# Optimization experiments

Measured on AMD Instinct MI355X. Metric: run time of the kernel, lower is better.

The kernel has to match this reference:

```python
import math
import jax, jax.numpy as jnp
import numpy as np

L, D, H, DFF, T, B, BUCKETS = 4, 512, 8, 2048, 256, 8, 32
DH = D // H


def _ln(x, g, b, eps=1e-6):
    m = x.mean(-1, keepdims=True)
    v = ((x - m) ** 2).mean(-1, keepdims=True)
    return (x - m) / jnp.sqrt(v + eps) * g + b


def setup_inputs() -> dict:
    key = jax.random.key(0)
    ki = iter(jax.random.split(key, 32))
    p = lambda shape: jax.random.normal(next(ki), shape, jnp.float32) * 0.02
    inp = {}
    inp['src'] = jax.random.normal(next(ki), (T, B, D), jnp.float32)
    inp['lengths'] = jax.random.randint(next(ki), (B,), 128, T + 1)
    inp['distances'] = jax.random.randint(next(ki), (B, T, T), 0, BUCKETS + 1)
    inp['u'] = jax.random.normal(next(ki), (D,), jnp.float32)
    inp['v'] = jax.random.normal(next(ki), (D,), jnp.float32)
    inp['ln1_g'] = jnp.ones((L, D)); inp['ln1_b'] = jnp.zeros((L, D))
    for nm in ['Wq', 'Wk', 'Wv', 'Wo']:
        inp[nm] = p((L, D, D))
    for nm in ['bq', 'bk', 'bv', 'bo']:
        inp[nm] = jnp.zeros((L, D))
    # learned relative-position embedding table per layer, padding row zeroed
    inp['rel_table'] = p((L, BUCKETS + 1, D)).at[:, BUCKETS, :].set(0.0)
    inp['ffn_ln_g'] = jnp.ones((L, D)); inp['ffn_ln_b'] = jnp.zeros((L, D))
    inp['W1'] = p((L, DFF, D)); inp['b1'] = jnp.zeros((L, DFF))
    inp['W2'] = p((L, D, DFF)); inp['b2'] = jnp.zeros((L, D))
    inp['final_ln_g'] = jnp.ones((D,)); inp['final_ln_b'] = jnp.zeros((D,))
    return inp


def reference(src, lengths, distances, u, v, ln1_g, ln1_b, Wq, bq, Wk, bk, Wv, bv,
              Wo, bo, rel_table, ffn_ln_g, ffn_ln_b, W1, b1, W2, b2,
              final_ln_g, final_ln_b):
    # onmt-style sinusoidal positional encoding with sqrt(d_model) scaling
    pos = jnp.arange(T, dtype=jnp.float32)[:, None]
    div = jnp.exp(jnp.arange(0, D, 2, dtype=jnp.float32) * (-math.log(10000.0) / D))
    pe = jnp.zeros((T, D)).at[:, 0::2].set(jnp.sin(pos * div)).at[:, 1::2].set(jnp.cos(pos * div))
    x = (src * math.sqrt(D) + pe[:, None, :]).transpose(1, 0, 2)  # (B,T,D)
    pad = jnp.arange(T)[None, :] >= lengths[:, None]  # (B,T), True = masked key
    uh = u.reshape(1, H, 1, DH)
    vh = v.reshape(1, H, 1, DH)
    for l in range(L):
        h = _ln(x, ln1_g[l], ln1_b[l])
        def heads(w, b_):
            return (h @ w.T + b_).reshape(B, T, H, DH).transpose(0, 2, 1, 3)
        q = heads(Wq[l], bq[l]) / math.sqrt(DH)  # (B,H,T,DH)
        k = heads(Wk[l], bk[l])
        val = heads(Wv[l], bv[l])
        # content term a_c = (q + u) k^T
        a_c = jnp.einsum('bhqd,bhkd->bhqk', q + uh, k)
        # relative term b_d = (q + v) R^T, R gathered per (query,key) pair
        rel = rel_table[l][distances].reshape(B, T, T, H, DH)  # (B,Q,K,H,DH)
        b_d = jnp.einsum('bhqd,bqkhd->bhqk', q + vh, rel)
        scores = (a_c + b_d).astype(jnp.float32)
        scores = jnp.where(pad[:, None, None, :], -1e18, scores)
        attn = jax.nn.softmax(scores, axis=-1)
        ctx = jnp.einsum('bhqk,bhkd->bhqd', attn, val)
        ctx = ctx.transpose(0, 2, 1, 3).reshape(B, T, D)
        out = ctx @ Wo[l].T + bo[l] + x  # residual (dropout=0)
        # PositionwiseFeedForward: LN -> W1 -> relu -> W2 -> +residual
        h2 = _ln(out, ffn_ln_g[l], ffn_ln_b[l])
        x = jax.nn.relu(h2 @ W1[l].T + b1[l]) @ W2[l].T + b2[l] + out
    x = _ln(x, final_ln_g, final_ln_b)
    return x.transpose(1, 0, 2)  # (T,B,D)
```

## Files before the change

### kernel.cpp

```cpp
#include <hip/hip_runtime.h>
#include <hip/hip_bf16.h>
#include <math.h>

constexpr int L = 4, D = 512, H = 8, DFF = 2048, T = 256, B = 8, BUCKETS = 32;
constexpr int DH = D / H;
constexpr int NT = B * T;
constexpr int QKVLD = 3 * D;

typedef __attribute__((ext_vector_type(8))) short bf16x8;
typedef __attribute__((ext_vector_type(4))) float f32x4;

__device__ __forceinline__ unsigned short f2bf(float f) {
    unsigned int x = __float_as_uint(f);
    return (unsigned short)((x + 0x7fffu + ((x >> 16) & 1u)) >> 16);
}
__device__ __forceinline__ float bf2f(unsigned short u) {
    return __uint_as_float((unsigned int)u << 16);
}

__device__ __forceinline__ void stage16(const unsigned short* g, short* l) {
    __builtin_amdgcn_global_load_lds((const __attribute__((address_space(1))) unsigned int*)g,
                                     (__attribute__((address_space(3))) unsigned int*)l,
                                     16, 0, 0);
}

__global__ __launch_bounds__(256) void embed_kernel(const float* __restrict__ src,
                                                    float* __restrict__ x)
{
    int t = blockIdx.x, tid = threadIdx.x;
    float pe0, pe1;
    {
        int d0 = tid, d1 = tid + 256;
        float dv0 = expf(-(float)(2 * (d0 >> 1)) * (9.210340371976184f / (float)D));
        float dv1 = expf(-(float)(2 * (d1 >> 1)) * (9.210340371976184f / (float)D));
        float a0 = (float)t * dv0, a1 = (float)t * dv1;
        pe0 = (d0 & 1) ? cosf(a0) : sinf(a0);
        pe1 = (d1 & 1) ? cosf(a1) : sinf(a1);
    }
#pragma unroll
    for (int b = 0; b < B; b++) {
        const float* sp = src + ((size_t)t * B + b) * D;
        float* xp = x + ((size_t)(b * T + t)) * D;
        xp[tid]       = sp[tid]       * 22.62741699796952f + pe0;
        xp[tid + 256] = sp[tid + 256] * 22.62741699796952f + pe1;
    }
}

__device__ __forceinline__ void ln_vals(float v0, float v1,
                                        const float* __restrict__ g,
                                        const float* __restrict__ bb,
                                        float* o0, float* o1, int tid)
{
    float s = v0 + v1, q2 = v0 * v0 + v1 * v1;
#pragma unroll
    for (int o = 32; o; o >>= 1) { s += __shfl_xor(s, o); q2 += __shfl_xor(q2, o); }
    __shared__ float rs[4], rq[4];
    int lane = tid & 63, wid = tid >> 6;
    if (lane == 0) { rs[wid] = s; rq[wid] = q2; }
    __syncthreads();
    s = rs[0] + rs[1] + rs[2] + rs[3];
    q2 = rq[0] + rq[1] + rq[2] + rq[3];
    float mean = s * (1.f / (float)D);
    float var = q2 * (1.f / (float)D) - mean * mean;
    float rstd = rsqrtf(var + 1e-6f);
    *o0 = (v0 - mean) * rstd * g[tid] + bb[tid];
    *o1 = (v1 - mean) * rstd * g[tid + 256] + bb[tid + 256];
}

__global__ __launch_bounds__(256) void ln_kernel(const float* __restrict__ x,
                                                 unsigned short* __restrict__ y,
                                                 const float* __restrict__ g,
                                                 const float* __restrict__ bb)
{
    int row = blockIdx.x, tid = threadIdx.x;
    float v0 = x[(size_t)row * D + tid], v1 = x[(size_t)row * D + tid + 256];
    float o0, o1;
    ln_vals(v0, v1, g, bb, &o0, &o1, tid);
    y[(size_t)row * D + tid] = f2bf(o0);
    y[(size_t)row * D + tid + 256] = f2bf(o1);
}

__global__ __launch_bounds__(256) void lnr_kernel(float* __restrict__ X,
                                                  const float* __restrict__ P,
                                                  const float* __restrict__ bias,
                                                  unsigned short* __restrict__ y,
                                                  const float* __restrict__ g,
                                                  const float* __restrict__ bb)
{
    int row = blockIdx.x, tid = threadIdx.x;
    float v0 = X[(size_t)row * D + tid] + bias[tid];
    float v1 = X[(size_t)row * D + tid + 256] + bias[tid + 256];
#pragma unroll
    for (int s = 0; s < 4; s++) {
        v0 += P[((size_t)s * NT + row) * D + tid];
        v1 += P[((size_t)s * NT + row) * D + tid + 256];
    }
    X[(size_t)row * D + tid] = v0;
    X[(size_t)row * D + tid + 256] = v1;
    float o0, o1;
    ln_vals(v0, v1, g, bb, &o0, &o1, tid);
    y[(size_t)row * D + tid] = f2bf(o0);
    y[(size_t)row * D + tid + 256] = f2bf(o1);
}

__global__ __launch_bounds__(256) void final_lnr_kernel(const float* __restrict__ X,
                                                        const float* __restrict__ P,
                                                        const float* __restrict__ bias,
                                                        float* __restrict__ out,
                                                        const float* __restrict__ g,
                                                        const float* __restrict__ bb)
{
    int row = blockIdx.x, tid = threadIdx.x;
    int b = row >> 8, t = row & (T - 1);
    float v0 = X[(size_t)row * D + tid] + bias[tid];
    float v1 = X[(size_t)row * D + tid + 256] + bias[tid + 256];
#pragma unroll
    for (int s = 0; s < 4; s++) {
        v0 += P[((size_t)s * NT + row) * D + tid];
        v1 += P[((size_t)s * NT + row) * D + tid + 256];
    }
    float o0, o1;
    ln_vals(v0, v1, g, bb, &o0, &o1, tid);
    float* op = out + ((size_t)t * B + b) * D;
    op[tid] = o0;
    op[tid + 256] = o1;
}

__global__ __launch_bounds__(256) void convert_all_kernel(
    const float* __restrict__ Wq, const float* __restrict__ Wk, const float* __restrict__ Wv,
    const float* __restrict__ Wo, const float* __restrict__ W1, const float* __restrict__ W2,
    const float* __restrict__ bq, const float* __restrict__ bk, const float* __restrict__ bv,
    const float* __restrict__ rel,
    unsigned short* __restrict__ WQKVb, unsigned short* __restrict__ Wob,
    unsigned short* __restrict__ W1b, unsigned short* __restrict__ W2b,
    unsigned short* __restrict__ relb,
    float* __restrict__ bqkv)
{
    int l = blockIdx.y;
    int g = blockIdx.x * 256 + threadIdx.x;
    const float* src; unsigned short* dst;
    bool zero = false;
    if (g < 98304) {
        int e = g * 8; int piece = e >> 18; int rem = e & 262143;
        src = (piece == 0 ? Wq : piece == 1 ? Wk : Wv) + (size_t)l * 262144 + rem;
        dst = WQKVb + (size_t)l * 786432 + e;
    } else if (g < 131072) {
        int e = (g - 98304) * 8;
        src = Wo + (size_t)l * 262144 + e; dst = Wob + (size_t)l * 262144 + e;
    } else if (g < 262144) {
        int e = (g - 131072) * 8;
        src = W1 + (size_t)l * 1048576 + e; dst = W1b + (size_t)l * 1048576 + e;
    } else if (g < 393216) {
        int e = (g - 262144) * 8;
        src = W2 + (size_t)l * 1048576 + e; dst = W2b + (size_t)l * 1048576 + e;
    } else {
        int e = (g - 393216) * 8;
        int row = e >> 9, cc = e & 511;
        dst = relb + (size_t)l * 24576 + e;
        if (row < BUCKETS + 1) src = rel + ((size_t)l * (BUCKETS + 1) + row) * 512 + cc;
        else { src = nullptr; zero = true; }
    }
    uint4 o;
    if (zero) { o.x = o.y = o.z = o.w = 0u; }
    else {
        float4 x = *(const float4*)src, y = *(const float4*)(src + 4);
        o.x = (unsigned)f2bf(x.x) | ((unsigned)f2bf(x.y) << 16);
        o.y = (unsigned)f2bf(x.z) | ((unsigned)f2bf(x.w) << 16);
        o.z = (unsigned)f2bf(y.x) | ((unsigned)f2bf(y.y) << 16);
        o.w = (unsigned)f2bf(y.z) | ((unsigned)f2bf(y.w) << 16);
    }
    *(uint4*)dst = o;
    if (g < 3 * D) {
        int piece = g >> 9, r2 = g & 511;
        bqkv[l * 1536 + g] = (piece == 0 ? bq : piece == 1 ? bk : bv)[l * 512 + r2];
    }
}

template <bool RELU, bool OUTBF16>
__global__ __launch_bounds__(256) void mgemm_kernel(
    const unsigned short* __restrict__ A,
    const unsigned short* __restrict__ W,
    const float* __restrict__ bias,
    void* __restrict__ Cv,
    int N, int M, int K)
{
    __shared__ short smA[2][128 * 32];
    __shared__ short smB[2][128 * 32];
    int tid = threadIdx.x;
    int bn = blockIdx.y * 128;
    int bm = blockIdx.x * 128;
    const unsigned short* Ab = A + (size_t)bn * K;
    const unsigned short* Wb = W + (size_t)bm * K;

    f32x4 acc[4][4];
#pragma unroll
    for (int i = 0; i < 4; i++)
#pragma unroll
        for (int j = 0; j < 4; j++) acc[i][j] = (f32x4){0.f, 0.f, 0.f, 0.f};

    const int c0 = tid, c1 = tid + 256;
    const int r0 = c0 >> 2, p0 = c0 & 3, l0 = p0 ^ ((r0 >> 1) & 3);
    const int r1 = c1 >> 2, p1 = c1 & 3, l1 = p1 ^ ((r1 >> 1) & 3);

    auto stage = [&](int buf, int k0) {
        stage16(Ab + (size_t)r0 * K + k0 + l0 * 8, &smA[buf][c0 * 8]);
        stage16(Ab + (size_t)r1 * K + k0 + l1 * 8, &smA[buf][c1 * 8]);
        stage16(Wb + (size_t)r0 * K + k0 + l0 * 8, &smB[buf][c0 * 8]);
        stage16(Wb + (size_t)r1 * K + k0 + l1 * 8, &smB[buf][c1 * 8]);
    };

    const int lane = tid & 63;
    const int wv = tid >> 6, wr = wv >> 1, wc = wv & 1;
    int aoff[4], boff[4];
#pragma unroll
    for (int i = 0; i < 4; i++) {
        int ra = wr * 64 + i * 16 + (lane & 15);
        int ca = (lane >> 4) ^ ((ra >> 1) & 3);
        aoff[i] = ra * 32 + ca * 8;
        int rb = wc * 64 + i * 16 + (lane & 15);
        int cb = (lane >> 4) ^ ((rb >> 1) & 3);
        boff[i] = rb * 32 + cb * 8;
    }

    stage(0, 0);
    const int nkt = K >> 5;
    for (int kt = 0; kt < nkt; ++kt) {
        __syncthreads();
        int cur = kt & 1;
        if (kt + 1 < nkt) stage(cur ^ 1, (kt + 1) << 5);
        const short* sa = smA[cur];
        const short* sb = smB[cur];
        bf16x8 af[4], bfr[4];
#pragma unroll
        for (int i = 0; i < 4; i++) af[i] = *(const bf16x8*)(sa + aoff[i]);
#pragma unroll
        for (int j = 0; j < 4; j++) bfr[j] = *(const bf16x8*)(sb + boff[j]);
#pragma unroll
        for (int i = 0; i < 4; i++)
#pragma unroll
            for (int j = 0; j < 4; j++)
                acc[i][j] = __builtin_amdgcn_mfma_f32_16x16x32_bf16(af[i], bfr[j], acc[i][j], 0, 0, 0);
    }

#pragma unroll
    for (int j = 0; j < 4; j++) {
        int col = bm + wc * 64 + j * 16 + (lane & 15);
        float bval = bias[col];
#pragma unroll
        for (int i = 0; i < 4; i++) {
            f32x4 v = acc[i][j];
#pragma unroll
            for (int r = 0; r < 4; r++) {
                int row = bn + wr * 64 + i * 16 + (lane >> 4) * 4 + r;
                float val = v[r] + bval;
                if (RELU) val = fmaxf(val, 0.f);
                if (OUTBF16) ((unsigned short*)Cv)[(size_t)row * M + col] = f2bf(val);
                else         ((float*)Cv)[(size_t)row * M + col] = val;
            }
        }
    }
}

__global__ __launch_bounds__(256) void mgemm_splitk_kernel(
    const unsigned short* __restrict__ A,
    const unsigned short* __restrict__ W,
    float* __restrict__ P,
    int N, int M, int K, int Ksub)
{
    __shared__ short smA[2][128 * 32];
    __shared__ short smB[2][128 * 32];
    int tid = threadIdx.x;
    int s = blockIdx.z;
    int bn = blockIdx.y * 128;
    int bm = blockIdx.x * 128;
    const unsigned short* Ab = A + (size_t)bn * K + s * Ksub;
    const unsigned short* Wb = W + (size_t)bm * K + s * Ksub;

    f32x4 acc[4][4];
#pragma unroll
    for (int i = 0; i < 4; i++)
#pragma unroll
        for (int j = 0; j < 4; j++) acc[i][j] = (f32x4){0.f, 0.f, 0.f, 0.f};

    const int c0 = tid, c1 = tid + 256;
    const int r0 = c0 >> 2, p0 = c0 & 3, l0 = p0 ^ ((r0 >> 1) & 3);
    const int r1 = c1 >> 2, p1 = c1 & 3, l1 = p1 ^ ((r1 >> 1) & 3);

    auto stage = [&](int buf, int k0) {
        stage16(Ab + (size_t)r0 * K + k0 + l0 * 8, &smA[buf][c0 * 8]);
        stage16(Ab + (size_t)r1 * K + k0 + l1 * 8, &smA[buf][c1 * 8]);
        stage16(Wb + (size_t)r0 * K + k0 + l0 * 8, &smB[buf][c0 * 8]);
        stage16(Wb + (size_t)r1 * K + k0 + l1 * 8, &smB[buf][c1 * 8]);
    };

    const int lane = tid & 63;
    const int wv = tid >> 6, wr = wv >> 1, wc = wv & 1;
    int aoff[4], boff[4];
#pragma unroll
    for (int i = 0; i < 4; i++) {
        int ra = wr * 64 + i * 16 + (lane & 15);
        int ca = (lane >> 4) ^ ((ra >> 1) & 3);
        aoff[i] = ra * 32 + ca * 8;
        int rb = wc * 64 + i * 16 + (lane & 15);
        int cb = (lane >> 4) ^ ((rb >> 1) & 3);
        boff[i] = rb * 32 + cb * 8;
    }

    stage(0, 0);
    const int nkt = Ksub >> 5;
    for (int kt = 0; kt < nkt; ++kt) {
        __syncthreads();
        int cur = kt & 1;
        if (kt + 1 < nkt) stage(cur ^ 1, (kt + 1) << 5);
        const short* sa = smA[cur];
        const short* sb = smB[cur];
        bf16x8 af[4], bfr[4];
#pragma unroll
        for (int i = 0; i < 4; i++) af[i] = *(const bf16x8*)(sa + aoff[i]);
#pragma unroll
        for (int j = 0; j < 4; j++) bfr[j] = *(const bf16x8*)(sb + boff[j]);
#pragma unroll
        for (int i = 0; i < 4; i++)
#pragma unroll
            for (int j = 0; j < 4; j++)
                acc[i][j] = __builtin_amdgcn_mfma_f32_16x16x32_bf16(af[i], bfr[j], acc[i][j], 0, 0, 0);
    }

#pragma unroll
    for (int j = 0; j < 4; j++) {
        int col = bm + wc * 64 + j * 16 + (lane & 15);
#pragma unroll
        for (int i = 0; i < 4; i++) {
            f32x4 v = acc[i][j];
#pragma unroll
            for (int r = 0; r < 4; r++) {
                int row = bn + wr * 64 + i * 16 + (lane >> 4) * 4 + r;
                P[((size_t)s * N + row) * M + col] = v[r];
            }
        }
    }
}

__global__ __launch_bounds__(256) void vtrans_kernel(const unsigned short* __restrict__ qkv,
                                                     unsigned short* __restrict__ vt)
{
    __shared__ unsigned short tile[64 * 66];
    int bh = blockIdx.x, b = bh >> 3, h = bh & 7;
    int kc = blockIdx.y * 64;
    int tid = threadIdx.x;
    int r = tid >> 2, c0 = (tid & 3) * 16;
    const unsigned short* rp = qkv + (size_t)(b * T + kc + r) * QKVLD + 2 * D + h * 64 + c0;
    uint4 w0 = *(const uint4*)rp;
    uint4 w1 = *(const uint4*)(rp + 8);
    unsigned short* tp = &tile[r * 66 + c0];
    unsigned int ww[8] = {w0.x, w0.y, w0.z, w0.w, w1.x, w1.y, w1.z, w1.w};
#pragma unroll
    for (int e = 0; e < 8; e++) {
        tp[2 * e]     = (unsigned short)(ww[e] & 0xffffu);
        tp[2 * e + 1] = (unsigned short)(ww[e] >> 16);
    }
    __syncthreads();
    int d = tid >> 2, k0 = (tid & 3) * 16;
    unsigned int outw[8];
#pragma unroll
    for (int i = 0; i < 8; i++) {
        unsigned int lo = tile[(k0 + 2 * i) * 66 + d];
        unsigned int hi = tile[(k0 + 2 * i + 1) * 66 + d];
        outw[i] = lo | (hi << 16);
    }
    unsigned short* op = vt + (size_t)(bh * 64 + d) * 256 + kc + k0;
    *(uint4*)op = *(uint4*)&outw[0];
    *(uint4*)(op + 8) = *(uint4*)&outw[4];
}

__global__ __launch_bounds__(256) void fattn_kernel(
    const unsigned short* __restrict__ qkv,
    const unsigned short* __restrict__ vt,
    const unsigned short* __restrict__ relb,
    const float* __restrict__ uvec,
    const float* __restrict__ vvec,
    const int* __restrict__ dist,
    const int* __restrict__ lengths,
    unsigned short* __restrict__ ctx)
{
    __shared__ unsigned short Ps[4][16][256];
    __shared__ float Qrel[4][16][49];

    int bh = blockIdx.x, b = bh >> 3, h = bh & 7;
    int qi0 = blockIdx.y * 64;
    int tid = threadIdx.x, w = tid >> 6, lane = tid & 63;
    int l15 = lane & 15, g = lane >> 4;
    int qr = qi0 + w * 16;

    const unsigned short* qbase = qkv + (size_t)(b * T + qr + l15) * QKVLD + h * 64 + g * 8;
    bf16x8 qa0 = *(const bf16x8*)(qbase);
    bf16x8 qa1 = *(const bf16x8*)(qbase + 32);

    bf16x8 qu0, qu1;
    {
        const float* up = uvec + h * 64 + g * 8;
        float ua0[8], ua1[8];
        *(float4*)&ua0[0] = *(const float4*)(up);
        *(float4*)&ua0[4] = *(const float4*)(up + 4);
        *(float4*)&ua1[0] = *(const float4*)(up + 32);
        *(float4*)&ua1[4] = *(const float4*)(up + 36);
#pragma unroll
        for (int e = 0; e < 8; e++) {
            qu0[e] = (short)f2bf(0.125f * bf2f((unsigned short)qa0[e]) + ua0[e]);
            qu1[e] = (short)f2bf(0.125f * bf2f((unsigned short)qa1[e]) + ua1[e]);
        }
    }

    {
        const float* vp = vvec + h * 64 + g * 8;
        float va0[8], va1[8];
        *(float4*)&va0[0] = *(const float4*)(vp);
        *(float4*)&va0[4] = *(const float4*)(vp + 4);
        *(float4*)&va1[0] = *(const float4*)(vp + 32);
        *(float4*)&va1[4] = *(const float4*)(vp + 36);
        bf16x8 qh0, qh1;
#pragma unroll
        for (int e = 0; e < 8; e++) {
            qh0[e] = (short)f2bf(0.125f * bf2f((unsigned short)qa0[e]) + va0[e]);
            qh1[e] = (short)f2bf(0.125f * bf2f((unsigned short)qa1[e]) + va1[e]);
        }
        f32x4 qacc[3];
#pragma unroll
        for (int j = 0; j < 3; j++) qacc[j] = (f32x4){0.f, 0.f, 0.f, 0.f};
#pragma unroll
        for (int j = 0; j < 3; j++) {
            const unsigned short* rp = relb + (size_t)(j * 16 + l15) * 512 + h * 64 + g * 8;
            bf16x8 r0 = *(const bf16x8*)(rp);
            bf16x8 r1 = *(const bf16x8*)(rp + 32);
            qacc[j] = __builtin_amdgcn_mfma_f32_16x16x32_bf16(qh0, r0, qacc[j], 0, 0, 0);
            qacc[j] = __builtin_amdgcn_mfma_f32_16x16x32_bf16(qh1, r1, qacc[j], 0, 0, 0);
        }
#pragma unroll
        for (int j = 0; j < 3; j++)
#pragma unroll
            for (int r = 0; r < 4; r++)
                Qrel[w][g * 4 + r][j * 16 + l15] = qacc[j][r];
    }

    f32x4 acc[16];
#pragma unroll
    for (int j = 0; j < 16; j++) acc[j] = (f32x4){0.f, 0.f, 0.f, 0.f};
    const unsigned short* kbase = qkv + (size_t)(b * T) * QKVLD + 512 + h * 64 + g * 8;
#pragma unroll
    for (int j = 0; j < 16; j++) {
        const unsigned short* kp = kbase + (size_t)(j * 16 + l15) * QKVLD;
        bf16x8 k0 = *(const bf16x8*)(kp);
        bf16x8 k1 = *(const bf16x8*)(kp + 32);
        acc[j] = __builtin_amdgcn_mfma_f32_16x16x32_bf16(qu0, k0, acc[j], 0, 0, 0);
        acc[j] = __builtin_amdgcn_mfma_f32_16x16x32_bf16(qu1, k1, acc[j], 0, 0, 0);
    }

    int len = lengths[b];
    float rinv[4];
    const int* db = dist + (size_t)b * T * T;
#pragma unroll
    for (int r = 0; r < 4; r++) {
        int rowloc = g * 4 + r;
        int qrow = qr + rowloc;
        const int* dpr = db + (size_t)qrow * T;
        float m = -3.0e38f;
#pragma unroll
        for (int j = 0; j < 16; j++) {
            int ki = j * 16 + l15;
            int dv = dpr[ki];
            float s = acc[j][r] + Qrel[w][rowloc][dv];
            s = (ki < len) ? s : -1.0e30f;
            acc[j][r] = s;
            m = fmaxf(m, s);
        }
#pragma unroll
        for (int o = 8; o; o >>= 1) m = fmaxf(m, __shfl_xor(m, o));
        float sum = 0.f;
#pragma unroll
        for (int j = 0; j < 16; j++) {
            int ki = j * 16 + l15;
            float p = __expf(acc[j][r] - m);
            sum += p;
            int cph = ((ki >> 3) ^ (rowloc & 7));
            Ps[w][rowloc][cph * 8 + (ki & 7)] = f2bf(p);
        }
#pragma unroll
        for (int o = 8; o; o >>= 1) sum += __shfl_xor(sum, o);
        rinv[r] = 1.0f / sum;
    }

    f32x4 oacc[4];
#pragma unroll
    for (int j = 0; j < 4; j++) oacc[j] = (f32x4){0.f, 0.f, 0.f, 0.f};
    const unsigned short* vtb = vt + (size_t)bh * 64 * 256;
#pragma unroll
    for (int ks = 0; ks < 8; ks++) {
        int c = ks * 4 + g;
        int cph = c ^ (l15 & 7);
        bf16x8 pa = *(const bf16x8*)&Ps[w][l15][cph * 8];
#pragma unroll
        for (int j2 = 0; j2 < 4; j2++) {
            bf16x8 vb = *(const bf16x8*)(vtb + (size_t)(j2 * 16 + l15) * 256 + c * 8);
            oacc[j2] = __builtin_amdgcn_mfma_f32_16x16x32_bf16(pa, vb, oacc[j2], 0, 0, 0);
        }
    }

#pragma unroll
    for (int j2 = 0; j2 < 4; j2++) {
#pragma unroll
        for (int r = 0; r < 4; r++) {
            int qrow = qr + g * 4 + r;
            int dcol = j2 * 16 + l15;
            ctx[(size_t)(b * T + qrow) * D + h * 64 + dcol] = f2bf(oacc[j2][r] * rinv[r]);
        }
    }
}

extern "C" void kernel_launch(void* const* d_in, const int* in_sizes, int n_in,
                              void* d_out, int out_size, void* d_ws, size_t ws_size,
                              hipStream_t stream)
{
    const float* src     = (const float*)d_in[0];
    const int*   lengths = (const int*)d_in[1];
    const int*   dist    = (const int*)d_in[2];
    const float* u       = (const float*)d_in[3];
    const float* v       = (const float*)d_in[4];
    const float* ln1_g   = (const float*)d_in[5];
    const float* ln1_b   = (const float*)d_in[6];
    const float* Wq      = (const float*)d_in[7];
    const float* Wk      = (const float*)d_in[8];
    const float* Wv      = (const float*)d_in[9];
    const float* Wo      = (const float*)d_in[10];
    const float* bq      = (const float*)d_in[11];
    const float* bk      = (const float*)d_in[12];
    const float* bv      = (const float*)d_in[13];
    const float* bo      = (const float*)d_in[14];
    const float* rel     = (const float*)d_in[15];
    const float* fg      = (const float*)d_in[16];
    const float* fb      = (const float*)d_in[17];
    const float* W1      = (const float*)d_in[18];
    const float* b1      = (const float*)d_in[19];
    const float* W2      = (const float*)d_in[20];
    const float* b2      = (const float*)d_in[21];
    const float* flg     = (const float*)d_in[22];
    const float* flb     = (const float*)d_in[23];

    float* ws = (float*)d_ws;
    float*          X     = ws;
    unsigned short* QKVb  = (unsigned short*)(ws + 1048576);
    unsigned short* Hb    = (unsigned short*)(ws + 2621440);
    unsigned short* CTX   = (unsigned short*)(ws + 3145728);
    unsigned short* FF1   = (unsigned short*)(ws + 3670016);
    unsigned short* VT    = (unsigned short*)(ws + 5767168);
    float*          Pbuf  = ws + 6291456;
    unsigned short* WQKVb = (unsigned short*)(ws + 10485760);
    unsigned short* Wob   = (unsigned short*)(ws + 12058624);
    unsigned short* W1b   = (unsigned short*)(ws + 12582912);
    unsigned short* W2b   = (unsigned short*)(ws + 14680064);
    unsigned short* RELb  = (unsigned short*)(ws + 16777216);
    float*          bqkv  = ws + 16826368;

    embed_kernel<<<T, 256, 0, stream>>>(src, X);

    convert_all_kernel<<<dim3(1548, L), 256, 0, stream>>>(
        Wq, Wk, Wv, Wo, W1, W2, bq, bk, bv, rel,
        WQKVb, Wob, W1b, W2b, RELb, bqkv);

    for (int l = 0; l < L; l++) {
        const unsigned short* wqkv = WQKVb + (size_t)l * 786432;
        const unsigned short* wob  = Wob   + (size_t)l * 262144;
        const unsigned short* w1b  = W1b   + (size_t)l * 1048576;
        const unsigned short* w2b  = W2b   + (size_t)l * 1048576;
        const unsigned short* relb = RELb  + (size_t)l * 24576;
        const float*          bql  = bqkv  + (size_t)l * 1536;

        if (l == 0)
            ln_kernel<<<NT, 256, 0, stream>>>(X, Hb, ln1_g, ln1_b);
        else
            lnr_kernel<<<NT, 256, 0, stream>>>(X, Pbuf, b2 + (size_t)(l - 1) * D,
                                               Hb, ln1_g + l * D, ln1_b + l * D);

        mgemm_kernel<false, true><<<dim3(12, 16), 256, 0, stream>>>(
            Hb, wqkv, bql, QKVb, NT, QKVLD, D);

        vtrans_kernel<<<dim3(64, 4), 256, 0, stream>>>(QKVb, VT);

        fattn_kernel<<<dim3(B * H, T / 64), 256, 0, stream>>>(
            QKVb, VT, relb, u, v, dist, lengths, CTX);

        mgemm_splitk_kernel<<<dim3(4, 16, 4), 256, 0, stream>>>(
            CTX, wob, Pbuf, NT, D, D, D / 4);

        lnr_kernel<<<NT, 256, 0, stream>>>(X, Pbuf, bo + (size_t)l * D,
                                           Hb, fg + l * D, fb + l * D);

        mgemm_kernel<true, true><<<dim3(16, 16), 256, 0, stream>>>(
            Hb, w1b, b1 + (size_t)l * DFF, FF1, NT, DFF, D);

        mgemm_splitk_kernel<<<dim3(4, 16, 4), 256, 0, stream>>>(
            FF1, w2b, Pbuf, NT, D, DFF, DFF / 4);
    }

    final_lnr_kernel<<<NT, 256, 0, stream>>>(X, Pbuf, b2 + (size_t)(L - 1) * D,
                                             (float*)d_out, flg, flb);
}
```

Before: 521.8 us.

## Fuse the whole encoder into one cooperative persistent megakernel with grid syncs

Replaces the per-layer sequence of separate kernel launches (LN, QKV GEMM, V transpose, attention, split-K GEMMs) with a single cooperative kernel of 256 blocks. Each stage runs as a device function over work units, with grid.sync between stages. The goal is to remove launch overhead and inter-kernel gaps, at the cost of grid-wide barriers and a fixed 256-block grid that may underuse the GPU in some stages. It falls back to the old multi-kernel path if the cooperative launch fails.

```diff
diff --git a/kernel.cpp b/kernel.cpp
--- a/kernel.cpp
+++ b/kernel.cpp
@@ -1,6 +1,9 @@
 #include <hip/hip_runtime.h>
+#include <hip/hip_cooperative_groups.h>
 #include <hip/hip_bf16.h>
 #include <math.h>
+
+namespace cg = cooperative_groups;
 
 constexpr int L = 4, D = 512, H = 8, DFF = 2048, T = 256, B = 8, BUCKETS = 32;
 constexpr int DH = D / H;
@@ -23,6 +26,7 @@
                                      (__attribute__((address_space(3))) unsigned int*)l,
                                      16, 0, 0);
 }
+
 
 __global__ __launch_bounds__(256) void embed_kernel(const float* __restrict__ src,
                                                     float* __restrict__ x)
@@ -46,10 +50,10 @@
     }
 }
 
-__device__ __forceinline__ void ln_vals(float v0, float v1,
-                                        const float* __restrict__ g,
-                                        const float* __restrict__ bb,
-                                        float* o0, float* o1, int tid)
+__device__ __forceinline__ void ln_vals_k(float v0, float v1,
+                                          const float* __restrict__ g,
+                                          const float* __restrict__ bb,
+                                          float* o0, float* o1, int tid)
 {
     float s = v0 + v1, q2 = v0 * v0 + v1 * v1;
 #pragma unroll
@@ -75,7 +79,7 @@
     int row = blockIdx.x, tid = threadIdx.x;
     float v0 = x[(size_t)row * D + tid], v1 = x[(size_t)row * D + tid + 256];
     float o0, o1;
-    ln_vals(v0, v1, g, bb, &o0, &o1, tid);
+    ln_vals_k(v0, v1, g, bb, &o0, &o1, tid);
     y[(size_t)row * D + tid] = f2bf(o0);
     y[(size_t)row * D + tid + 256] = f2bf(o1);
 }
@@ -98,7 +102,7 @@
     X[(size_t)row * D + tid] = v0;
     X[(size_t)row * D + tid + 256] = v1;
     float o0, o1;
-    ln_vals(v0, v1, g, bb, &o0, &o1, tid);
+    ln_vals_k(v0, v1, g, bb, &o0, &o1, tid);
     y[(size_t)row * D + tid] = f2bf(o0);
     y[(size_t)row * D + tid + 256] = f2bf(o1);
 }
@@ -120,7 +124,7 @@
         v1 += P[((size_t)s * NT + row) * D + tid + 256];
     }
     float o0, o1;
-    ln_vals(v0, v1, g, bb, &o0, &o1, tid);
+    ln_vals_k(v0, v1, g, bb, &o0, &o1, tid);
     float* op = out + ((size_t)t * B + b) * D;
     op[tid] = o0;
     op[tid + 256] = o1;
@@ -335,7 +339,7 @@
 #pragma unroll
             for (int r = 0; r < 4; r++) {
                 int row = bn + wr * 64 + i * 16 + (lane >> 4) * 4 + r;
-                P[((size_t)s * N + row) * M + col] = v[r];
+                P[((size_t)s * NT + row) * M + col] = v[r];
             }
         }
     }
@@ -430,10 +434,10 @@
 #pragma unroll
         for (int j = 0; j < 3; j++) {
             const unsigned short* rp = relb + (size_t)(j * 16 + l15) * 512 + h * 64 + g * 8;
-            bf16x8 r0 = *(const bf16x8*)(rp);
-            bf16x8 r1 = *(const bf16x8*)(rp + 32);
-            qacc[j] = __builtin_amdgcn_mfma_f32_16x16x32_bf16(qh0, r0, qacc[j], 0, 0, 0);
-            qacc[j] = __builtin_amdgcn_mfma_f32_16x16x32_bf16(qh1, r1, qacc[j], 0, 0, 0);
+            bf16x8 rr0 = *(const bf16x8*)(rp);
+            bf16x8 rr1 = *(const bf16x8*)(rp + 32);
+            qacc[j] = __builtin_amdgcn_mfma_f32_16x16x32_bf16(qh0, rr0, qacc[j], 0, 0, 0);
+            qacc[j] = __builtin_amdgcn_mfma_f32_16x16x32_bf16(qh1, rr1, qacc[j], 0, 0, 0);
         }
 #pragma unroll
         for (int j = 0; j < 3; j++)
@@ -514,6 +518,499 @@
             ctx[(size_t)(b * T + qrow) * D + h * 64 + dcol] = f2bf(oacc[j2][r] * rinv[r]);
         }
     }
+}
+
+
+struct SMem {
+    union U {
+        struct { short A[2][4096]; short Bv[2][4096]; } g;
+        struct { unsigned short Ps[4][16][256]; float Qrel[4][16][49]; } at;
+        struct { unsigned short tile[64 * 66]; } vt;
+    } u;
+    float red[8];
+};
+
+struct MArgs {
+    const float* src; const int* lengths; const int* dist;
+    const float* uvec; const float* vvec;
+    const float* ln1_g; const float* ln1_b;
+    const float* bo; const float* fg; const float* fb;
+    const float* b1; const float* b2; const float* flg; const float* flb;
+    float* X; unsigned short* QKVb; unsigned short* Hb; unsigned short* CTX;
+    unsigned short* FF1; unsigned short* VT; float* Pbuf;
+    const unsigned short* WQKVb; const unsigned short* Wob;
+    const unsigned short* W1b; const unsigned short* W2b;
+    const unsigned short* RELb; const float* bqkv;
+    float* out;
+};
+
+__device__ __forceinline__ void ln_vals_m(float v0, float v1,
+                                          const float* __restrict__ g,
+                                          const float* __restrict__ bb,
+                                          float* o0, float* o1, int tid, float* red)
+{
+    float s = v0 + v1, q2 = v0 * v0 + v1 * v1;
+#pragma unroll
+    for (int o = 32; o; o >>= 1) { s += __shfl_xor(s, o); q2 += __shfl_xor(q2, o); }
+    int lane = tid & 63, wid = tid >> 6;
+    if (lane == 0) { red[wid] = s; red[4 + wid] = q2; }
+    __syncthreads();
+    s = red[0] + red[1] + red[2] + red[3];
+    q2 = red[4] + red[5] + red[6] + red[7];
+    __syncthreads();
+    float mean = s * (1.f / (float)D);
+    float var = q2 * (1.f / (float)D) - mean * mean;
+    float rstd = rsqrtf(var + 1e-6f);
+    *o0 = (v0 - mean) * rstd * g[tid] + bb[tid];
+    *o1 = (v1 - mean) * rstd * g[tid + 256] + bb[tid + 256];
+}
+
+__device__ void st_embed_ln(SMem* sm, const MArgs& a, int bid, int tid)
+{
+    int d0 = tid, d1 = tid + 256;
+    float dv0 = expf(-(float)(2 * (d0 >> 1)) * (9.210340371976184f / (float)D));
+    float dv1 = expf(-(float)(2 * (d1 >> 1)) * (9.210340371976184f / (float)D));
+    for (int i = 0; i < 8; i++) {
+        int row = bid * 8 + i;
+        int b = row >> 8, t = row & (T - 1);
+        float a0 = (float)t * dv0, a1 = (float)t * dv1;
+        float pe0 = (d0 & 1) ? cosf(a0) : sinf(a0);
+        float pe1 = (d1 & 1) ? cosf(a1) : sinf(a1);
+        const float* sp = a.src + ((size_t)t * B + b) * D;
+        float v0 = sp[d0] * 22.62741699796952f + pe0;
+        float v1 = sp[d1] * 22.62741699796952f + pe1;
+        a.X[(size_t)row * D + d0] = v0;
+        a.X[(size_t)row * D + d1] = v1;
+        float o0, o1;
+        ln_vals_m(v0, v1, a.ln1_g, a.ln1_b, &o0, &o1, tid, sm->red);
+        a.Hb[(size_t)row * D + d0] = f2bf(o0);
+        a.Hb[(size_t)row * D + d1] = f2bf(o1);
+    }
+}
+
+__device__ void st_lnr(SMem* sm, const MArgs& a, int bid, int tid,
+                       const float* __restrict__ bias,
+                       const float* __restrict__ g, const float* __restrict__ bb)
+{
+    for (int i = 0; i < 8; i++) {
+        int row = bid * 8 + i;
+        float v0 = a.X[(size_t)row * D + tid] + bias[tid];
+        float v1 = a.X[(size_t)row * D + tid + 256] + bias[tid + 256];
+#pragma unroll
+        for (int s = 0; s < 4; s++) {
+            v0 += a.Pbuf[((size_t)s * NT + row) * D + tid];
+            v1 += a.Pbuf[((size_t)s * NT + row) * D + tid + 256];
+        }
+        a.X[(size_t)row * D + tid] = v0;
+        a.X[(size_t)row * D + tid + 256] = v1;
+        float o0, o1;
+        ln_vals_m(v0, v1, g, bb, &o0, &o1, tid, sm->red);
+        a.Hb[(size_t)row * D + tid] = f2bf(o0);
+        a.Hb[(size_t)row * D + tid + 256] = f2bf(o1);
+    }
+}
+
+__device__ void st_final(SMem* sm, const MArgs& a, int bid, int tid)
+{
+    const float* bias = a.b2 + (size_t)(L - 1) * D;
+    for (int i = 0; i < 8; i++) {
+        int row = bid * 8 + i;
+        int b = row >> 8, t = row & (T - 1);
+        float v0 = a.X[(size_t)row * D + tid] + bias[tid];
+        float v1 = a.X[(size_t)row * D + tid + 256] + bias[tid + 256];
+#pragma unroll
+        for (int s = 0; s < 4; s++) {
+            v0 += a.Pbuf[((size_t)s * NT + row) * D + tid];
+            v1 += a.Pbuf[((size_t)s * NT + row) * D + tid + 256];
+        }
+        float o0, o1;
+        ln_vals_m(v0, v1, a.flg, a.flb, &o0, &o1, tid, sm->red);
+        float* op = a.out + ((size_t)t * B + b) * D;
+        op[tid] = o0;
+        op[tid + 256] = o1;
+    }
+}
+
+template <bool RELU>
+__device__ void st_gemm(SMem* sm, int unit, int tid,
+                        const unsigned short* __restrict__ A,
+                        const unsigned short* __restrict__ W,
+                        const float* __restrict__ bias,
+                        unsigned short* __restrict__ C,
+                        int M, int K, int tx, int ntiles)
+{
+    if (unit >= ntiles) return;
+    auto& G = sm->u.g;
+    int bm = (unit % tx) * 128, bn = (unit / tx) * 128;
+    const unsigned short* Ab = A + (size_t)bn * K;
+    const unsigned short* Wb = W + (size_t)bm * K;
+
+    f32x4 acc[4][4];
+#pragma unroll
+    for (int i = 0; i < 4; i++)
+#pragma unroll
+        for (int j = 0; j < 4; j++) acc[i][j] = (f32x4){0.f, 0.f, 0.f, 0.f};
+
+    const int c0 = tid, c1 = tid + 256;
+    const int r0 = c0 >> 2, p0 = c0 & 3, l0 = p0 ^ ((r0 >> 1) & 3);
+    const int r1 = c1 >> 2, p1 = c1 & 3, l1 = p1 ^ ((r1 >> 1) & 3);
+
+    auto stage = [&](int buf, int k0) {
+        stage16(Ab + (size_t)r0 * K + k0 + l0 * 8, &G.A[buf][c0 * 8]);
+        stage16(Ab + (size_t)r1 * K + k0 + l1 * 8, &G.A[buf][c1 * 8]);
+        stage16(Wb + (size_t)r0 * K + k0 + l0 * 8, &G.Bv[buf][c0 * 8]);
+        stage16(Wb + (size_t)r1 * K + k0 + l1 * 8, &G.Bv[buf][c1 * 8]);
+    };
+
+    const int lane = tid & 63;
+    const int wv = tid >> 6, wr = wv >> 1, wc = wv & 1;
+    int aoff[4], boff[4];
+#pragma unroll
+    for (int i = 0; i < 4; i++) {
+        int ra = wr * 64 + i * 16 + (lane & 15);
+        int ca = (lane >> 4) ^ ((ra >> 1) & 3);
+        aoff[i] = ra * 32 + ca * 8;
+        int rb = wc * 64 + i * 16 + (lane & 15);
+        int cb = (lane >> 4) ^ ((rb >> 1) & 3);
+        boff[i] = rb * 32 + cb * 8;
+    }
+
+    stage(0, 0);
+    const int nkt = K >> 5;
+    for (int kt = 0; kt < nkt; ++kt) {
+        __syncthreads();
+        int cur = kt & 1;
+        if (kt + 1 < nkt) stage(cur ^ 1, (kt + 1) << 5);
+        const short* sa = G.A[cur];
+        const short* sb = G.Bv[cur];
+        bf16x8 af[4], bfr[4];
+#pragma unroll
+        for (int i = 0; i < 4; i++) af[i] = *(const bf16x8*)(sa + aoff[i]);
+#pragma unroll
+        for (int j = 0; j < 4; j++) bfr[j] = *(const bf16x8*)(sb + boff[j]);
+#pragma unroll
+        for (int i = 0; i < 4; i++)
+#pragma unroll
+            for (int j = 0; j < 4; j++)
+                acc[i][j] = __builtin_amdgcn_mfma_f32_16x16x32_bf16(af[i], bfr[j], acc[i][j], 0, 0, 0);
+    }
+
+#pragma unroll
+    for (int j = 0; j < 4; j++) {
+        int col = bm + wc * 64 + j * 16 + (lane & 15);
+        float bval = bias[col];
+#pragma unroll
+        for (int i = 0; i < 4; i++) {
+            f32x4 v = acc[i][j];
+#pragma unroll
+            for (int r = 0; r < 4; r++) {
+                int row = bn + wr * 64 + i * 16 + (lane >> 4) * 4 + r;
+                float val = v[r] + bval;
+                if (RELU) val = fmaxf(val, 0.f);
+                C[(size_t)row * M + col] = f2bf(val);
+            }
+        }
+    }
+}
+
+__device__ void st_gemm_sk(SMem* sm, int unit, int tid,
+                           const unsigned short* __restrict__ A,
+                           const unsigned short* __restrict__ W,
+                           float* __restrict__ P,
+                           int M, int K, int Ksub)
+{
+    auto& G = sm->u.g;
+    int s = unit >> 6, rem = unit & 63;
+    int bm = (rem & 3) * 128, bn = (rem >> 2) * 128;
+    const unsigned short* Ab = A + (size_t)bn * K + s * Ksub;
+    const unsigned short* Wb = W + (size_t)bm * K + s * Ksub;
+
+    f32x4 acc[4][4];
+#pragma unroll
+    for (int i = 0; i < 4; i++)
+#pragma unroll
+        for (int j = 0; j < 4; j++) acc[i][j] = (f32x4){0.f, 0.f, 0.f, 0.f};
+
+    const int c0 = tid, c1 = tid + 256;
+    const int r0 = c0 >> 2, p0 = c0 & 3, l0 = p0 ^ ((r0 >> 1) & 3);
+    const int r1 = c1 >> 2, p1 = c1 & 3, l1 = p1 ^ ((r1 >> 1) & 3);
+
+    auto stage = [&](int buf, int k0) {
+        stage16(Ab + (size_t)r0 * K + k0 + l0 * 8, &G.A[buf][c0 * 8]);
+        stage16(Ab + (size_t)r1 * K + k0 + l1 * 8, &G.A[buf][c1 * 8]);
+        stage16(Wb + (size_t)r0 * K + k0 + l0 * 8, &G.Bv[buf][c0 * 8]);
+        stage16(Wb + (size_t)r1 * K + k0 + l1 * 8, &G.Bv[buf][c1 * 8]);
+    };
+
+    const int lane = tid & 63;
+    const int wv = tid >> 6, wr = wv >> 1, wc = wv & 1;
+    int aoff[4], boff[4];
+#pragma unroll
+    for (int i = 0; i < 4; i++) {
+        int ra = wr * 64 + i * 16 + (lane & 15);
+        int ca = (lane >> 4) ^ ((ra >> 1) & 3);
+        aoff[i] = ra * 32 + ca * 8;
+        int rb = wc * 64 + i * 16 + (lane & 15);
+        int cb = (lane >> 4) ^ ((rb >> 1) & 3);
+        boff[i] = rb * 32 + cb * 8;
+    }
+
+    stage(0, 0);
+    const int nkt = Ksub >> 5;
+    for (int kt = 0; kt < nkt; ++kt) {
+        __syncthreads();
+        int cur = kt & 1;
+        if (kt + 1 < nkt) stage(cur ^ 1, (kt + 1) << 5);
+        const short* sa = G.A[cur];
+        const short* sb = G.Bv[cur];
+        bf16x8 af[4], bfr[4];
+#pragma unroll
+        for (int i = 0; i < 4; i++) af[i] = *(const bf16x8*)(sa + aoff[i]);
+#pragma unroll
+        for (int j = 0; j < 4; j++) bfr[j] = *(const bf16x8*)(sb + boff[j]);
+#pragma unroll
+        for (int i = 0; i < 4; i++)
+#pragma unroll
+            for (int j = 0; j < 4; j++)
+                acc[i][j] = __builtin_amdgcn_mfma_f32_16x16x32_bf16(af[i], bfr[j], acc[i][j], 0, 0, 0);
+    }
+
+#pragma unroll
+    for (int j = 0; j < 4; j++) {
+        int col = bm + wc * 64 + j * 16 + (lane & 15);
+#pragma unroll
+        for (int i = 0; i < 4; i++) {
+            f32x4 v = acc[i][j];
+#pragma unroll
+            for (int r = 0; r < 4; r++) {
+                int row = bn + wr * 64 + i * 16 + (lane >> 4) * 4 + r;
+                P[((size_t)s * NT + row) * M + col] = v[r];
+            }
+        }
+    }
+}
+
+__device__ void st_vtrans(SMem* sm, int unit, int tid,
+                          const unsigned short* __restrict__ qkv,
+                          unsigned short* __restrict__ vt)
+{
+    unsigned short* tile = sm->u.vt.tile;
+    int bh = unit & 63, b = bh >> 3, h = bh & 7;
+    int kc = (unit >> 6) * 64;
+    int r = tid >> 2, c0 = (tid & 3) * 16;
+    const unsigned short* rp = qkv + (size_t)(b * T + kc + r) * QKVLD + 2 * D + h * 64 + c0;
+    uint4 w0 = *(const uint4*)rp;
+    uint4 w1 = *(const uint4*)(rp + 8);
+    unsigned short* tp = &tile[r * 66 + c0];
+    unsigned int ww[8] = {w0.x, w0.y, w0.z, w0.w, w1.x, w1.y, w1.z, w1.w};
+#pragma unroll
+    for (int e = 0; e < 8; e++) {
+        tp[2 * e]     = (unsigned short)(ww[e] & 0xffffu);
+        tp[2 * e + 1] = (unsigned short)(ww[e] >> 16);
+    }
+    __syncthreads();
+    int d = tid >> 2, k0 = (tid & 3) * 16;
+    unsigned int outw[8];
+#pragma unroll
+    for (int i = 0; i < 8; i++) {
+        unsigned int lo = tile[(k0 + 2 * i) * 66 + d];
+        unsigned int hi = tile[(k0 + 2 * i + 1) * 66 + d];
+        outw[i] = lo | (hi << 16);
+    }
+    unsigned short* op = vt + (size_t)(bh * 64 + d) * 256 + kc + k0;
+    *(uint4*)op = *(uint4*)&outw[0];
+    *(uint4*)(op + 8) = *(uint4*)&outw[4];
+    __syncthreads();
+}
+
+__device__ void st_fattn(SMem* sm, int unit, int tid,
+                         const unsigned short* __restrict__ qkv,
+                         const unsigned short* __restrict__ vt,
+                         const unsigned short* __restrict__ relb,
+                         const float* __restrict__ uvec,
+                         const float* __restrict__ vvec,
+                         const int* __restrict__ dist,
+                         const int* __restrict__ lengths,
+                         unsigned short* __restrict__ ctx)
+{
+    auto& AT = sm->u.at;
+    int bh = unit & 63, b = bh >> 3, h = bh & 7;
+    int qi0 = (unit >> 6) * 64;
+    int w = tid >> 6, lane = tid & 63;
+    int l15 = lane & 15, g = lane >> 4;
+    int qr = qi0 + w * 16;
+
+    const unsigned short* qbase = qkv + (size_t)(b * T + qr + l15) * QKVLD + h * 64 + g * 8;
+    bf16x8 qa0 = *(const bf16x8*)(qbase);
+    bf16x8 qa1 = *(const bf16x8*)(qbase + 32);
+
+    bf16x8 qu0, qu1;
+    {
+        const float* up = uvec + h * 64 + g * 8;
+        float ua0[8], ua1[8];
+        *(float4*)&ua0[0] = *(const float4*)(up);
+        *(float4*)&ua0[4] = *(const float4*)(up + 4);
+        *(float4*)&ua1[0] = *(const float4*)(up + 32);
+        *(float4*)&ua1[4] = *(const float4*)(up + 36);
+#pragma unroll
+        for (int e = 0; e < 8; e++) {
+            qu0[e] = (short)f2bf(0.125f * bf2f((unsigned short)qa0[e]) + ua0[e]);
+            qu1[e] = (short)f2bf(0.125f * bf2f((unsigned short)qa1[e]) + ua1[e]);
+        }
+    }
+
+    {
+        const float* vp = vvec + h * 64 + g * 8;
+        float va0[8], va1[8];
+        *(float4*)&va0[0] = *(const float4*)(vp);
+        *(float4*)&va0[4] = *(const float4*)(vp + 4);
+        *(float4*)&va1[0] = *(const float4*)(vp + 32);
+        *(float4*)&va1[4] = *(const float4*)(vp + 36);
+        bf16x8 qh0, qh1;
+#pragma unroll
+        for (int e = 0; e < 8; e++) {
+            qh0[e] = (short)f2bf(0.125f * bf2f((unsigned short)qa0[e]) + va0[e]);
+            qh1[e] = (short)f2bf(0.125f * bf2f((unsigned short)qa1[e]) + va1[e]);
+        }
+        f32x4 qacc[3];
+#pragma unroll
+        for (int j = 0; j < 3; j++) qacc[j] = (f32x4){0.f, 0.f, 0.f, 0.f};
+#pragma unroll
+        for (int j = 0; j < 3; j++) {
+            const unsigned short* rp = relb + (size_t)(j * 16 + l15) * 512 + h * 64 + g * 8;
+            bf16x8 rr0 = *(const bf16x8*)(rp);
+            bf16x8 rr1 = *(const bf16x8*)(rp + 32);
+            qacc[j] = __builtin_amdgcn_mfma_f32_16x16x32_bf16(qh0, rr0, qacc[j], 0, 0, 0);
+            qacc[j] = __builtin_amdgcn_mfma_f32_16x16x32_bf16(qh1, rr1, qacc[j], 0, 0, 0);
+        }
+#pragma unroll
+        for (int j = 0; j < 3; j++)
+#pragma unroll
+            for (int r = 0; r < 4; r++)
+                AT.Qrel[w][g * 4 + r][j * 16 + l15] = qacc[j][r];
+    }
+
+    f32x4 acc[16];
+#pragma unroll
+    for (int j = 0; j < 16; j++) acc[j] = (f32x4){0.f, 0.f, 0.f, 0.f};
+    const unsigned short* kbase = qkv + (size_t)(b * T) * QKVLD + 512 + h * 64 + g * 8;
+#pragma unroll
+    for (int j = 0; j < 16; j++) {
+        const unsigned short* kp = kbase + (size_t)(j * 16 + l15) * QKVLD;
+        bf16x8 k0 = *(const bf16x8*)(kp);
+        bf16x8 k1 = *(const bf16x8*)(kp + 32);
+        acc[j] = __builtin_amdgcn_mfma_f32_16x16x32_bf16(qu0, k0, acc[j], 0, 0, 0);
+        acc[j] = __builtin_amdgcn_mfma_f32_16x16x32_bf16(qu1, k1, acc[j], 0, 0, 0);
+    }
+
+    int len = lengths[b];
+    float rinv[4];
+    const int* db = dist + (size_t)b * T * T;
+#pragma unroll
+    for (int r = 0; r < 4; r++) {
+        int rowloc = g * 4 + r;
+        int qrow = qr + rowloc;
+        const int* dpr = db + (size_t)qrow * T;
+        float m = -3.0e38f;
+#pragma unroll
+        for (int j = 0; j < 16; j++) {
+            int ki = j * 16 + l15;
+            int dv = dpr[ki];
+            float s = acc[j][r] + AT.Qrel[w][rowloc][dv];
+            s = (ki < len) ? s : -1.0e30f;
+            acc[j][r] = s;
+            m = fmaxf(m, s);
+        }
+#pragma unroll
+        for (int o = 8; o; o >>= 1) m = fmaxf(m, __shfl_xor(m, o));
+        float sum = 0.f;
+#pragma unroll
+        for (int j = 0; j < 16; j++) {
+            int ki = j * 16 + l15;
+            float p = __expf(acc[j][r] - m);
+            sum += p;
+            int cph = ((ki >> 3) ^ (rowloc & 7));
+            AT.Ps[w][rowloc][cph * 8 + (ki & 7)] = f2bf(p);
+        }
+#pragma unroll
+        for (int o = 8; o; o >>= 1) sum += __shfl_xor(sum, o);
+        rinv[r] = 1.0f / sum;
+    }
+
+    f32x4 oacc[4];
+#pragma unroll
+    for (int j = 0; j < 4; j++) oacc[j] = (f32x4){0.f, 0.f, 0.f, 0.f};
+    const unsigned short* vtb = vt + (size_t)bh * 64 * 256;
+#pragma unroll
+    for (int ks = 0; ks < 8; ks++) {
+        int c = ks * 4 + g;
+        int cph = c ^ (l15 & 7);
+        bf16x8 pa = *(const bf16x8*)&AT.Ps[w][l15][cph * 8];
+#pragma unroll
+        for (int j2 = 0; j2 < 4; j2++) {
+            bf16x8 vb = *(const bf16x8*)(vtb + (size_t)(j2 * 16 + l15) * 256 + c * 8);
+            oacc[j2] = __builtin_amdgcn_mfma_f32_16x16x32_bf16(pa, vb, oacc[j2], 0, 0, 0);
+        }
+    }
+
+#pragma unroll
+    for (int j2 = 0; j2 < 4; j2++) {
+#pragma unroll
+        for (int r = 0; r < 4; r++) {
+            int qrow = qr + g * 4 + r;
+            int dcol = j2 * 16 + l15;
+            ctx[(size_t)(b * T + qrow) * D + h * 64 + dcol] = f2bf(oacc[j2][r] * rinv[r]);
+        }
+    }
+}
+
+__global__ void __launch_bounds__(256) mega_kernel(MArgs a)
+{
+    __shared__ SMem sm;
+    cg::grid_group grid = cg::this_grid();
+    int bid = blockIdx.x, tid = threadIdx.x;
+
+    st_embed_ln(&sm, a, bid, tid);
+    grid.sync();
+
+    for (int l = 0; l < L; ++l) {
+        const unsigned short* wqkv = a.WQKVb + (size_t)l * 786432;
+        const unsigned short* wob  = a.Wob   + (size_t)l * 262144;
+        const unsigned short* w1b  = a.W1b   + (size_t)l * 1048576;
+        const unsigned short* w2b  = a.W2b   + (size_t)l * 1048576;
+        const unsigned short* relb = a.RELb  + (size_t)l * 24576;
+        const float*          bql  = a.bqkv  + (size_t)l * 1536;
+
+        st_gemm<false>(&sm, bid, tid, a.Hb, wqkv, bql, a.QKVb, QKVLD, D, 12, 192);
+        grid.sync();
+
+        st_vtrans(&sm, bid, tid, a.QKVb, a.VT);
+        grid.sync();
+
+        st_fattn(&sm, bid, tid, a.QKVb, a.VT, relb, a.uvec, a.vvec,
+                 a.dist, a.lengths, a.CTX);
+        grid.sync();
+
+        st_gemm_sk(&sm, bid, tid, a.CTX, wob, a.Pbuf, D, D, D / 4);
+        grid.sync();
+
+        st_lnr(&sm, a, bid, tid, a.bo + (size_t)l * D, a.fg + l * D, a.fb + l * D);
+        grid.sync();
+
+        st_gemm<true>(&sm, bid, tid, a.Hb, w1b, a.b1 + (size_t)l * DFF, a.FF1, DFF, D, 16, 256);
+        grid.sync();
+
+        st_gemm_sk(&sm, bid, tid, a.FF1, w2b, a.Pbuf, D, DFF, DFF / 4);
+        grid.sync();
+
+        if (l < L - 1) {
+            st_lnr(&sm, a, bid, tid, a.b2 + (size_t)l * D,
+                   a.ln1_g + (l + 1) * D, a.ln1_b + (l + 1) * D);
+            grid.sync();
+        }
+    }
+
+    st_final(&sm, a, bid, tid);
 }
 
 extern "C" void kernel_launch(void* const* d_in, const int* in_sizes, int n_in,
@@ -560,11 +1057,30 @@
     unsigned short* RELb  = (unsigned short*)(ws + 16777216);
     float*          bqkv  = ws + 16826368;
 
-    embed_kernel<<<T, 256, 0, stream>>>(src, X);
-
     convert_all_kernel<<<dim3(1548, L), 256, 0, stream>>>(
         Wq, Wk, Wv, Wo, W1, W2, bq, bk, bv, rel,
         WQKVb, Wob, W1b, W2b, RELb, bqkv);
+
+    MArgs a;
+    a.src = src; a.lengths = lengths; a.dist = dist;
+    a.uvec = u; a.vvec = v;
+    a.ln1_g = ln1_g; a.ln1_b = ln1_b;
+    a.bo = bo; a.fg = fg; a.fb = fb;
+    a.b1 = b1; a.b2 = b2; a.flg = flg; a.flb = flb;
+    a.X = X; a.QKVb = QKVb; a.Hb = Hb; a.CTX = CTX;
+    a.FF1 = FF1; a.VT = VT; a.Pbuf = Pbuf;
+    a.WQKVb = WQKVb; a.Wob = Wob; a.W1b = W1b; a.W2b = W2b;
+    a.RELb = RELb; a.bqkv = bqkv;
+    a.out = (float*)d_out;
+
+    void* kargs[] = { (void*)&a };
+    hipError_t err = hipLaunchCooperativeKernel((const void*)mega_kernel,
+                                                dim3(256), dim3(256),
+                                                kargs, 0, stream);
+    if (err == hipSuccess) return;
+    (void)hipGetLastError();
+
+    embed_kernel<<<T, 256, 0, stream>>>(src, X);
 
     for (int l = 0; l < L; l++) {
         const unsigned short* wqkv = WQKVb + (size_t)l * 786432;
```

Result: slower. 1.725 ms (+230.5%).
